# Kernel optimization log

Measured on AMD Instinct MI355X. Metric: run time of the kernel, lower is better.

Reference implementation:

```python
import jax, jax.numpy as jnp
import numpy as np

B, T, C, H = 4, 4096, 768, 64  # batch, seq, embed_size, head_size


def setup_inputs() -> dict:
    key = jax.random.key(0)
    kx, kq, kk, kv = jax.random.split(key, 4)
    s = 1.0 / np.sqrt(C)
    return {
        "x": jax.random.normal(kx, (B, T, C), dtype=jnp.float32),
        "Wq": jax.random.normal(kq, (C, H), dtype=jnp.float32) * s,
        "Wk": jax.random.normal(kk, (C, H), dtype=jnp.float32) * s,
        "Wv": jax.random.normal(kv, (C, H), dtype=jnp.float32) * s,
    }


def reference(x, Wq, Wk, Wv):
    Bx, Tx, Cx = x.shape
    Q = x @ Wq  # [B, T, H]
    K = x @ Wk
    V = x @ Wv
    # NOTE: original scales by sqrt(C) = sqrt(embed_size), not head_size
    scores = jnp.einsum('bqh,bkh->bqk', Q, K) / jnp.sqrt(jnp.asarray(Cx, x.dtype))
    causal = jnp.tril(jnp.ones((Tx, Tx), dtype=bool))
    scores = jnp.where(causal, scores, -jnp.inf)
    weights = jax.nn.softmax(scores, axis=-1)
    # dropout = identity in eval mode
    return jnp.einsum('bqk,bkh->bqh', weights, V)
```

## Files before the change

kernel.cpp:

```cpp
#include <hip/hip_runtime.h>

typedef __bf16 bf16x8 __attribute__((ext_vector_type(8)));
typedef float f32x4 __attribute__((ext_vector_type(4)));

#define MFMA16(a,b,c) __builtin_amdgcn_mfma_f32_16x16x32_bf16(a,b,c,0,0,0)

__device__ __forceinline__ unsigned short f2b(float x){
  __bf16 b = (__bf16)x;
  return __builtin_bit_cast(unsigned short, b);
}
__device__ __forceinline__ float b2f(unsigned short u){
  return __builtin_bit_cast(float, ((unsigned)u)<<16);
}

__device__ __forceinline__ void gld16(const void* g, void* l){
  __builtin_amdgcn_global_load_lds(
      (const __attribute__((address_space(1))) unsigned int*)g,
      (__attribute__((address_space(3))) unsigned int*)l, 16, 0, 0);
}

__global__ __launch_bounds__(256) void pack_w(const float* __restrict__ Wq,
                                              const float* __restrict__ Wk,
                                              const float* __restrict__ Wv,
                                              unsigned short* __restrict__ Wt){
  int idx = blockIdx.x*256 + threadIdx.x;
  int n = idx/768, c = idx - n*768;
  const float* W = (n < 64) ? Wq : ((n < 128) ? Wk : Wv);
  Wt[n*768 + c] = f2b(W[c*64 + (n & 63)]);
}

__global__ __launch_bounds__(256,2) void qkv_proj(const float* __restrict__ x,
                                                  const unsigned short* __restrict__ Wt,
                                                  unsigned short* __restrict__ Qb,
                                                  unsigned short* __restrict__ Kb,
                                                  unsigned short* __restrict__ Vt){
  __shared__ __attribute__((aligned(16))) float Xl[2][32*64];
  __shared__ __attribute__((aligned(16))) unsigned short Wl[2][192*64];
  const int tid = threadIdx.x;
  const int w = tid>>6, l = tid&63, quad = l>>4, lr = l&15;
  const int row0 = blockIdx.x*32;

  auto stage = [&](int kk, int buf){
#pragma unroll
    for(int i=0;i<2;i++){
      int n = (w*2+i)*4 + (l>>4);
      int sc = (l&15) ^ (n&15);
      gld16(x + (size_t)(row0+n)*768 + kk*64 + sc*4, &Xl[buf][(w*2+i)*256]);
    }
#pragma unroll
    for(int i=0;i<6;i++){
      int gr0 = (w*6+i)*8;
      int n = gr0 + (l>>3);
      int sc = (l&7) ^ (l>>3);
      gld16(Wt + (size_t)n*768 + kk*64 + sc*8, &Wl[buf][gr0*64]);
    }
  };

  f32x4 acc[2][3];
#pragma unroll
  for(int mt=0;mt<2;mt++)
#pragma unroll
    for(int nt=0;nt<3;nt++) acc[mt][nt] = (f32x4)0.0f;

  stage(0, 0);
  int buf = 0;
  for(int kk=0; kk<12; kk++){
    __syncthreads();
    if(kk+1 < 12) stage(kk+1, buf^1);
    bf16x8 a[2][2];
#pragma unroll
    for(int mt=0;mt<2;mt++){
#pragma unroll
      for(int ks=0;ks<2;ks++){
        int c = ks*8 + quad*2;
        f32x4 v0 = *(const f32x4*)&Xl[buf][(mt*16+lr)*64 + ((c   ^ lr)&15)*4];
        f32x4 v1 = *(const f32x4*)&Xl[buf][(mt*16+lr)*64 + (((c+1)^ lr)&15)*4];
#pragma unroll
        for(int jj=0;jj<4;jj++){ a[mt][ks][jj] = (__bf16)v0[jj]; a[mt][ks][4+jj] = (__bf16)v1[jj]; }
      }
    }
#pragma unroll
    for(int nt=0;nt<3;nt++){
#pragma unroll
      for(int ks=0;ks<2;ks++){
        int n = w*48 + nt*16 + lr;
        int q = ks*4 + quad;
        bf16x8 bfr = *(const bf16x8*)&Wl[buf][n*64 + ((q ^ (lr&7))&7)*8];
#pragma unroll
        for(int mt=0;mt<2;mt++) acc[mt][nt] = MFMA16(a[mt][ks], bfr, acc[mt][nt]);
      }
    }
    buf ^= 1;
  }
  const int b_ = row0>>12;
  const float sc = 0.03608439182435161f;
#pragma unroll
  for(int mt=0;mt<2;mt++){
    const int t0 = (row0 & 4095) + mt*16 + quad*4;
#pragma unroll
    for(int nt=0;nt<3;nt++){
      int g = w*48 + nt*16 + lr;
      if(g < 64){
#pragma unroll
        for(int r=0;r<4;r++) Qb[((size_t)(b_*4096 + t0 + r))*64 + g] = f2b(acc[mt][nt][r]*sc);
      } else if(g < 128){
#pragma unroll
        for(int r=0;r<4;r++) Kb[((size_t)(b_*4096 + t0 + r))*64 + (g-64)] = f2b(acc[mt][nt][r]);
      } else {
        ushort4 pk;
        pk.x = f2b(acc[mt][nt][0]); pk.y = f2b(acc[mt][nt][1]);
        pk.z = f2b(acc[mt][nt][2]); pk.w = f2b(acc[mt][nt][3]);
        *(ushort4*)&Vt[((size_t)(b_*64 + (g-128)))*4096 + t0] = pk;
      }
    }
  }
}

__device__ __forceinline__ void attn_stage(const unsigned short* kbp, const unsigned short* vbp,
                                           int kt, int w, int r8, int cj,
                                           unsigned short* Kl, unsigned short* Vl){
#pragma unroll
  for(int i=0;i<2;i++){
    int row = w*16 + i*8 + r8;
    int gc = cj ^ r8;
    gld16(kbp + ((size_t)(kt*64 + row))*64 + gc*8, Kl + (w*16 + i*8)*64);
    gld16(vbp + ((size_t)row)*4096 + kt*64 + gc*8, Vl + (w*16 + i*8)*64);
  }
}

__global__ __launch_bounds__(256,2) void attn(const unsigned short* __restrict__ Qb,
                                              const unsigned short* __restrict__ Kb,
                                              const unsigned short* __restrict__ Vt,
                                              unsigned short* __restrict__ Opart,
                                              float* __restrict__ Rpart){
  __shared__ __attribute__((aligned(16))) unsigned short Kl[2][64*64];
  __shared__ __attribute__((aligned(16))) unsigned short Vl[2][64*64];
  __shared__ __attribute__((aligned(16))) unsigned short Pl[4][32*72];
  const int tid = threadIdx.x;
  const int w = tid>>6, l = tid&63, quad = l>>4, lr = l&15;
  const int xx = 143 - blockIdx.x;
  int i = 0, accu = 0;
  while(true){ int c = (i+4)>>2; if(accu + c > xx) break; accu += c; i++; }
  const int r = xx - accu;
  const int b = blockIdx.y;
  const int q0 = i*128;
  const int lo = r*8;
  const int hi = min(lo+8, 2*i+2);
  const int diag0 = 2*i;
  const int r8 = l>>3, cj = l&7;
  const int lx = lr & 7;
  bf16x8 aq[2][2];
#pragma unroll
  for(int m=0;m<2;m++){
    const unsigned short* qp = Qb + ((size_t)(b*4096 + q0 + w*32 + m*16 + lr))*64 + quad*8;
    aq[m][0] = *(const bf16x8*)qp;
    aq[m][1] = *(const bf16x8*)(qp + 32);
  }
  f32x4 o_[2][4];
#pragma unroll
  for(int m=0;m<2;m++)
#pragma unroll
    for(int nt=0;nt<4;nt++) o_[m][nt] = (f32x4)0.0f;
  float rs[2][4] = {{0.f,0.f,0.f,0.f},{0.f,0.f,0.f,0.f}};
  const unsigned short* kbp = Kb + ((size_t)b*4096)*64;
  const unsigned short* vbp = Vt + ((size_t)b*64)*4096;
  unsigned short* pw = &Pl[w][0];

  attn_stage(kbp, vbp, lo, w, r8, cj, Kl[0], Vl[0]);
  int cur = 0;
  for(int kt = lo; kt < hi; kt++){
    __syncthreads();
    if(kt+1 < hi) attn_stage(kbp, vbp, kt+1, w, r8, cj, Kl[cur^1], Vl[cur^1]);
    f32x4 s4[2][4];
#pragma unroll
    for(int ct=0;ct<4;ct++){
      int base = (ct*16+lr)*64;
      bf16x8 b0 = *(const bf16x8*)&Kl[cur][base + ((quad    ^ lx)<<3)];
      bf16x8 b1 = *(const bf16x8*)&Kl[cur][base + (((4+quad)^ lx)<<3)];
#pragma unroll
      for(int m=0;m<2;m++){
        f32x4 z = (f32x4)0.0f;
        z = MFMA16(aq[m][0], b0, z);
        s4[m][ct] = MFMA16(aq[m][1], b1, z);
      }
    }
    if(kt >= diag0){
#pragma unroll
      for(int m=0;m<2;m++){
        int qg = q0 + w*32 + m*16 + quad*4;
#pragma unroll
        for(int ct=0;ct<4;ct++){
          int kg = kt*64 + ct*16 + lr;
#pragma unroll
          for(int rr=0;rr<4;rr++){
            float p = (kg <= qg + rr) ? __expf(s4[m][ct][rr]) : 0.0f;
            rs[m][rr] += p;
            pw[(m*16+quad*4+rr)*72 + ct*16 + lr] = f2b(p);
          }
        }
      }
    } else {
#pragma unroll
      for(int m=0;m<2;m++){
#pragma unroll
        for(int ct=0;ct<4;ct++){
#pragma unroll
          for(int rr=0;rr<4;rr++){
            float p = __expf(s4[m][ct][rr]);
            rs[m][rr] += p;
            pw[(m*16+quad*4+rr)*72 + ct*16 + lr] = f2b(p);
          }
        }
      }
    }
#pragma unroll
    for(int ks=0;ks<2;ks++){
      bf16x8 ap[2];
#pragma unroll
      for(int m=0;m<2;m++) ap[m] = *(const bf16x8*)&pw[(m*16+lr)*72 + ks*32 + quad*8];
#pragma unroll
      for(int nt=0;nt<4;nt++){
        bf16x8 bv = *(const bf16x8*)&Vl[cur][(nt*16+lr)*64 + (((ks*4+quad)^lx)<<3)];
#pragma unroll
        for(int m=0;m<2;m++) o_[m][nt] = MFMA16(ap[m], bv, o_[m][nt]);
      }
    }
    cur ^= 1;
  }
  const int slab = r*4 + b;
#pragma unroll
  for(int m=0;m<2;m++){
#pragma unroll
    for(int rr=0;rr<4;rr++){
      float t = rs[m][rr];
#pragma unroll
      for(int off=1; off<16; off<<=1) t += __shfl_xor(t, off, 16);
      int row = q0 + w*32 + m*16 + quad*4 + rr;
      if(lr == 0) Rpart[slab*4096 + row] = t;
#pragma unroll
      for(int nt=0;nt<4;nt++)
        Opart[((size_t)(slab*4096 + row))*64 + nt*16 + lr] = f2b(o_[m][nt][rr]);
    }
  }
}

__global__ __launch_bounds__(256) void combine(const unsigned short* __restrict__ Opart,
                                               const float* __restrict__ Rpart,
                                               float* __restrict__ out){
  int gid = blockIdx.x*256 + threadIdx.x;
  int cg = gid & 15;
  int t  = (gid >> 4) & 4095;
  int b  = gid >> 16;
  int i  = t >> 7;
  int np = (i + 4) >> 2;
  float o0=0.f, o1=0.f, o2=0.f, o3=0.f, rsum=0.f;
  for(int r=0; r<np; r++){
    int slab = r*4 + b;
    rsum += Rpart[slab*4096 + t];
    ushort4 u = *(const ushort4*)(Opart + ((size_t)(slab*4096 + t))*64 + cg*4);
    o0 += b2f(u.x); o1 += b2f(u.y); o2 += b2f(u.z); o3 += b2f(u.w);
  }
  float inv = 1.0f/rsum;
  f32x4 v; v[0]=o0*inv; v[1]=o1*inv; v[2]=o2*inv; v[3]=o3*inv;
  *(f32x4*)(out + ((size_t)(b*4096 + t))*64 + cg*4) = v;
}

extern "C" void kernel_launch(void* const* d_in, const int* in_sizes, int n_in,
                              void* d_out, int out_size, void* d_ws, size_t ws_size,
                              hipStream_t stream){
  const float* x  = (const float*)d_in[0];
  const float* Wq = (const float*)d_in[1];
  const float* Wk = (const float*)d_in[2];
  const float* Wv = (const float*)d_in[3];
  float* out = (float*)d_out;
  char* ws = (char*)d_ws;
  unsigned short* Wt = (unsigned short*)(ws);
  unsigned short* Qb = (unsigned short*)(ws + 0x080000);
  unsigned short* Kb = (unsigned short*)(ws + 0x280000);
  unsigned short* Vt = (unsigned short*)(ws + 0x480000);
  unsigned short* Opart = (unsigned short*)(ws + 0x680000);
  float* Rpart = (float*)(ws + 0x1680000);
  hipLaunchKernelGGL(pack_w,   dim3(576),     dim3(256), 0, stream, Wq, Wk, Wv, Wt);
  hipLaunchKernelGGL(qkv_proj, dim3(512),     dim3(256), 0, stream, x, Wt, Qb, Kb, Vt);
  hipLaunchKernelGGL(attn,     dim3(144, 4),  dim3(256), 0, stream, Qb, Kb, Vt, Opart, Rpart);
  hipLaunchKernelGGL(combine,  dim3(1024),    dim3(256), 0, stream, Opart, Rpart, out);
}
```

Measured before the change: 129.1 us.

## Keep softmax probabilities in registers via transposed QK and permlane swaps

Swaps the QK^T MFMA operands so each lane holds scores for a single query row. The probabilities are then converted with packed bf16 conversion and rearranged with permlane32/16 swaps straight into the A-operand layout for the PV MFMA. This removes the per-wave LDS P buffer and its store/load round trip. It also folds log2(e) into the Q scale so exp2 can replace expf, simplifies the row-sum reduction, and raises launch bounds to 3 blocks per CU now that LDS use is smaller. The risks are register pressure at higher occupancy and correctness of the lane permutation.

```diff
diff --git a/kernel.cpp b/kernel.cpp
--- a/kernel.cpp
+++ b/kernel.cpp
@@ -2,6 +2,7 @@
 
 typedef __bf16 bf16x8 __attribute__((ext_vector_type(8)));
 typedef float f32x4 __attribute__((ext_vector_type(4)));
+typedef unsigned int u32x4 __attribute__((ext_vector_type(4)));
 
 #define MFMA16(a,b,c) __builtin_amdgcn_mfma_f32_16x16x32_bf16(a,b,c,0,0,0)
 
@@ -11,6 +12,11 @@
 }
 __device__ __forceinline__ float b2f(unsigned short u){
   return __builtin_bit_cast(float, ((unsigned)u)<<16);
+}
+__device__ __forceinline__ unsigned cvtpk(float lo, float hi){
+  unsigned r;
+  asm("v_cvt_pk_bf16_f32 %0, %1, %2" : "=v"(r) : "v"(lo), "v"(hi));
+  return r;
 }
 
 __device__ __forceinline__ void gld16(const void* g, void* l){
@@ -93,7 +99,7 @@
     buf ^= 1;
   }
   const int b_ = row0>>12;
-  const float sc = 0.03608439182435161f;
+  const float sc = (float)(1.4426950408889634 * 0.03608439182435161);
 #pragma unroll
   for(int mt=0;mt<2;mt++){
     const int t0 = (row0 & 4095) + mt*16 + quad*4;
@@ -128,14 +134,13 @@
   }
 }
 
-__global__ __launch_bounds__(256,2) void attn(const unsigned short* __restrict__ Qb,
+__global__ __launch_bounds__(256,3) void attn(const unsigned short* __restrict__ Qb,
                                               const unsigned short* __restrict__ Kb,
                                               const unsigned short* __restrict__ Vt,
                                               unsigned short* __restrict__ Opart,
                                               float* __restrict__ Rpart){
   __shared__ __attribute__((aligned(16))) unsigned short Kl[2][64*64];
   __shared__ __attribute__((aligned(16))) unsigned short Vl[2][64*64];
-  __shared__ __attribute__((aligned(16))) unsigned short Pl[4][32*72];
   const int tid = threadIdx.x;
   const int w = tid>>6, l = tid&63, quad = l>>4, lr = l&15;
   const int xx = 143 - blockIdx.x;
@@ -161,10 +166,9 @@
   for(int m=0;m<2;m++)
 #pragma unroll
     for(int nt=0;nt<4;nt++) o_[m][nt] = (f32x4)0.0f;
-  float rs[2][4] = {{0.f,0.f,0.f,0.f},{0.f,0.f,0.f,0.f}};
+  float rs[2] = {0.f, 0.f};
   const unsigned short* kbp = Kb + ((size_t)b*4096)*64;
   const unsigned short* vbp = Vt + ((size_t)b*64)*4096;
-  unsigned short* pw = &Pl[w][0];
 
   attn_stage(kbp, vbp, lo, w, r8, cj, Kl[0], Vl[0]);
   int cur = 0;
@@ -175,27 +179,28 @@
 #pragma unroll
     for(int ct=0;ct<4;ct++){
       int base = (ct*16+lr)*64;
-      bf16x8 b0 = *(const bf16x8*)&Kl[cur][base + ((quad    ^ lx)<<3)];
-      bf16x8 b1 = *(const bf16x8*)&Kl[cur][base + (((4+quad)^ lx)<<3)];
+      bf16x8 k0 = *(const bf16x8*)&Kl[cur][base + ((quad    ^ lx)<<3)];
+      bf16x8 k1 = *(const bf16x8*)&Kl[cur][base + (((4+quad)^ lx)<<3)];
 #pragma unroll
       for(int m=0;m<2;m++){
         f32x4 z = (f32x4)0.0f;
-        z = MFMA16(aq[m][0], b0, z);
-        s4[m][ct] = MFMA16(aq[m][1], b1, z);
-      }
-    }
+        z = MFMA16(k0, aq[m][0], z);
+        s4[m][ct] = MFMA16(k1, aq[m][1], z);
+      }
+    }
+    float pv[2][4][4];
     if(kt >= diag0){
 #pragma unroll
       for(int m=0;m<2;m++){
-        int qg = q0 + w*32 + m*16 + quad*4;
+        int qg = q0 + w*32 + m*16 + lr;
 #pragma unroll
         for(int ct=0;ct<4;ct++){
-          int kg = kt*64 + ct*16 + lr;
+          int kg = kt*64 + ct*16 + quad*4;
 #pragma unroll
           for(int rr=0;rr<4;rr++){
-            float p = (kg <= qg + rr) ? __expf(s4[m][ct][rr]) : 0.0f;
-            rs[m][rr] += p;
-            pw[(m*16+quad*4+rr)*72 + ct*16 + lr] = f2b(p);
+            float p = (kg + rr <= qg) ? __builtin_exp2f(s4[m][ct][rr]) : 0.0f;
+            rs[m] += p;
+            pv[m][ct][rr] = p;
           }
         }
       }
@@ -206,23 +211,37 @@
         for(int ct=0;ct<4;ct++){
 #pragma unroll
           for(int rr=0;rr<4;rr++){
-            float p = __expf(s4[m][ct][rr]);
-            rs[m][rr] += p;
-            pw[(m*16+quad*4+rr)*72 + ct*16 + lr] = f2b(p);
+            float p = __builtin_exp2f(s4[m][ct][rr]);
+            rs[m] += p;
+            pv[m][ct][rr] = p;
           }
         }
       }
     }
+    bf16x8 ap[2][2];
+#pragma unroll
+    for(int m=0;m<2;m++){
+#pragma unroll
+      for(int ks=0;ks<2;ks++){
+        unsigned a0 = cvtpk(pv[m][2*ks  ][0], pv[m][2*ks  ][1]);
+        unsigned a1 = cvtpk(pv[m][2*ks  ][2], pv[m][2*ks  ][3]);
+        unsigned b0 = cvtpk(pv[m][2*ks+1][0], pv[m][2*ks+1][1]);
+        unsigned b1 = cvtpk(pv[m][2*ks+1][2], pv[m][2*ks+1][3]);
+        asm("v_permlane32_swap_b32 %0, %1" : "+v"(a0), "+v"(b0));
+        asm("v_permlane16_swap_b32 %0, %1" : "+v"(a0), "+v"(b0));
+        asm("v_permlane32_swap_b32 %0, %1" : "+v"(a1), "+v"(b1));
+        asm("v_permlane16_swap_b32 %0, %1" : "+v"(a1), "+v"(b1));
+        u32x4 wv; wv[0] = a0; wv[1] = a1; wv[2] = b0; wv[3] = b1;
+        ap[m][ks] = __builtin_bit_cast(bf16x8, wv);
+      }
+    }
 #pragma unroll
     for(int ks=0;ks<2;ks++){
-      bf16x8 ap[2];
-#pragma unroll
-      for(int m=0;m<2;m++) ap[m] = *(const bf16x8*)&pw[(m*16+lr)*72 + ks*32 + quad*8];
 #pragma unroll
       for(int nt=0;nt<4;nt++){
         bf16x8 bv = *(const bf16x8*)&Vl[cur][(nt*16+lr)*64 + (((ks*4+quad)^lx)<<3)];
 #pragma unroll
-        for(int m=0;m<2;m++) o_[m][nt] = MFMA16(ap[m], bv, o_[m][nt]);
+        for(int m=0;m<2;m++) o_[m][nt] = MFMA16(ap[m][ks], bv, o_[m][nt]);
       }
     }
     cur ^= 1;
@@ -230,13 +249,13 @@
   const int slab = r*4 + b;
 #pragma unroll
   for(int m=0;m<2;m++){
+    float t = rs[m];
+    t += __shfl_xor(t, 16);
+    t += __shfl_xor(t, 32);
+    if(quad == 0) Rpart[slab*4096 + q0 + w*32 + m*16 + lr] = t;
 #pragma unroll
     for(int rr=0;rr<4;rr++){
-      float t = rs[m][rr];
-#pragma unroll
-      for(int off=1; off<16; off<<=1) t += __shfl_xor(t, off, 16);
       int row = q0 + w*32 + m*16 + quad*4 + rr;
-      if(lr == 0) Rpart[slab*4096 + row] = t;
 #pragma unroll
       for(int nt=0;nt<4;nt++)
         Opart[((size_t)(slab*4096 + row))*64 + nt*16 + lr] = f2b(o_[m][nt][rr]);
```

New measurement: 131.7 us. About the same (+2.0%).
